# Kernel optimization log

Measured on AMD Instinct MI355X. Metric: run time of the kernel, lower is better.

## Reference

```python
import jax, jax.numpy as jnp
import numpy as np

N_NODES = 100000
N_EDGES = 3200000
D = 128
BN_EPS = 1e-5


def setup_inputs() -> dict:
    key = jax.random.key(0)
    k1, k2, k3, k4 = jax.random.split(key, 4)
    x = jax.random.normal(k1, (N_NODES, D), dtype=jnp.float32)
    edge_index = jax.random.randint(k2, (2, N_EDGES), 0, N_NODES, dtype=jnp.int64)
    # GCNConv linear weight, torch nn.Linear convention: [out_dim, in_dim]
    W = jax.random.normal(k3, (D, D), dtype=jnp.float32) * (1.0 / np.sqrt(D))
    # BatchNorm1d affine params
    gamma = jnp.ones((D,), dtype=jnp.float32) + 0.1 * jax.random.normal(k4, (D,), dtype=jnp.float32)
    beta = jnp.zeros((D,), dtype=jnp.float32)
    return {"x": x, "edge_index": edge_index, "W": W, "gamma": gamma, "beta": beta}


def reference(x, edge_index, W, gamma, beta):
    # GCNConv(bias=False, add_self_loops=False), then BN (batch stats), ReLU, skip-add.
    src, dst = edge_index[0], edge_index[1]
    n = x.shape[0]

    # linear transform: [N, D_out]
    h = x @ W.T

    # symmetric GCN normalization: deg over destination, norm = d^-1/2[src]*d^-1/2[dst]
    ones = jnp.ones((src.shape[0],), dtype=x.dtype)
    deg = jax.ops.segment_sum(ones, dst, num_segments=n)
    dinv = jnp.where(deg > 0, jax.lax.rsqrt(jnp.maximum(deg, 1.0)), 0.0)
    norm = dinv[src] * dinv[dst]  # [E]

    # gather-message-scatter: [E, D] -> [N, D]
    msg = h[src] * norm[:, None]
    agg = jax.ops.segment_sum(msg, dst, num_segments=n)

    # BatchNorm1d in training mode (batch statistics, biased variance)
    mean = jnp.mean(agg, axis=0)
    var = jnp.mean(jnp.square(agg - mean), axis=0)
    bn = (agg - mean) * jax.lax.rsqrt(var + BN_EPS) * gamma + beta

    # ReLU + residual skip (dims match)
    out = jax.nn.relu(bn) + x
    return out
```

## Files before the change

kernel.cpp:

```cpp
#include <hip/hip_runtime.h>
#include <hip/hip_bf16.h>
#include <cstdint>
#include <cstddef>

#define D 128
#define SBLK 512
#define SBBITS 10
#define NSB 128
#define TILE 2048

typedef __attribute__((ext_vector_type(8))) short short8;
typedef __attribute__((ext_vector_type(4))) float f32x4;

__device__ __forceinline__ unsigned short f2bf(float f) {
    union { float f; unsigned u; } v; v.f = f;
    unsigned r = v.u + 0x7FFF + ((v.u >> 16) & 1);
    return (unsigned short)(r >> 16);
}
__device__ __forceinline__ float bflo(unsigned p) {
    union { unsigned u; float f; } v; v.u = p << 16; return v.f;
}
__device__ __forceinline__ float bfhi(unsigned p) {
    union { unsigned u; float f; } v; v.u = p & 0xFFFF0000u; return v.f;
}

__global__ void k_detect(const unsigned* __restrict__ ei, int E, int* flag) {
    if (threadIdx.x == 0 && blockIdx.x == 0) {
        int n = E < 256 ? E : 256;
        int allz = 1;
        for (int k = 0; k < n; ++k) {
            if (ei[2 * k + 1] != 0u) { allz = 0; break; }
        }
        *flag = allz;
    }
}

__global__ void k_wcvt(const float* __restrict__ W, unsigned short* __restrict__ Wbf) {
    int i = blockIdx.x * 256 + threadIdx.x;
    if (i < D * D) Wbf[i] = f2bf(W[i]);
}

__global__ __launch_bounds__(256) void k_gemm(const float* __restrict__ x,
                                              const unsigned short* __restrict__ Wbf,
                                              unsigned short* __restrict__ h, int M) {
    int wave = threadIdx.x >> 6, lane = threadIdx.x & 63;
    int m0 = blockIdx.x * 64 + wave * 16;
    int lr = lane & 15;
    int lg = lane >> 4;
    f32x4 acc[8];
#pragma unroll
    for (int i = 0; i < 8; ++i) acc[i] = (f32x4){0.f, 0.f, 0.f, 0.f};

    int row = m0 + lr;
    int rowc = row < M ? row : M - 1;
    const float* xr = x + (size_t)rowc * D;

#pragma unroll
    for (int ks = 0; ks < 4; ++ks) {
        int k0 = ks * 32 + lg * 8;
        float4 a0 = *(const float4*)(xr + k0);
        float4 a1 = *(const float4*)(xr + k0 + 4);
        short8 af;
        af[0] = (short)f2bf(a0.x); af[1] = (short)f2bf(a0.y);
        af[2] = (short)f2bf(a0.z); af[3] = (short)f2bf(a0.w);
        af[4] = (short)f2bf(a1.x); af[5] = (short)f2bf(a1.y);
        af[6] = (short)f2bf(a1.z); af[7] = (short)f2bf(a1.w);
#pragma unroll
        for (int nt = 0; nt < 8; ++nt) {
            short8 bf = *(const short8*)(Wbf + (size_t)(nt * 16 + lr) * D + k0);
            acc[nt] = __builtin_amdgcn_mfma_f32_16x16x32_bf16(af, bf, acc[nt], 0, 0, 0);
        }
    }
#pragma unroll
    for (int nt = 0; nt < 8; ++nt) {
#pragma unroll
        for (int r = 0; r < 4; ++r) {
            int rr = m0 + lg * 4 + r;
            if (rr < M) h[(size_t)rr * D + nt * 16 + lr] = f2bf(acc[nt][r]);
        }
    }
}

__global__ __launch_bounds__(256) void k_bin(const int* __restrict__ ei, int E,
                                             const int* __restrict__ flagp,
                                             int* __restrict__ g_sbcnt,
                                             unsigned* __restrict__ binned, int C2) {
    __shared__ unsigned stage[TILE];
    __shared__ unsigned char ssb[TILE];
    __shared__ int hcnt[NSB], hoff[NSB], lcur[NSB], gbase[NSB];
    int f64 = *flagp;
    int t = threadIdx.x;
    int base = blockIdx.x * TILE;
    int cnt = E - base; if (cnt > TILE) cnt = TILE;

    if (t < NSB) hcnt[t] = 0;
    __syncthreads();

    unsigned ent[8]; int esb[8];
#pragma unroll
    for (int j = 0; j < 8; ++j) {
        int idx = j * 256 + t;
        esb[j] = -1;
        if (idx < cnt) {
            int e = base + idx;
            int s, d;
            if (f64) { s = ei[2 * e]; d = ei[2 * (E + e)]; }
            else     { s = ei[e];     d = ei[E + e]; }
            esb[j] = d >> SBBITS;
            ent[j] = (unsigned)s | ((unsigned)(d & ((1 << SBBITS) - 1)) << 17);
            atomicAdd(&hcnt[esb[j]], 1);
        }
    }
    __syncthreads();
    if (t < NSB) hoff[t] = hcnt[t];
    __syncthreads();
#pragma unroll
    for (int off = 1; off < NSB; off <<= 1) {
        int a = (t < NSB && t >= off) ? hoff[t - off] : 0;
        __syncthreads();
        if (t < NSB) hoff[t] += a;
        __syncthreads();
    }
    if (t < NSB) {
        int ex = hoff[t] - hcnt[t];
        lcur[t] = ex;
        hoff[t] = ex;
        gbase[t] = (hcnt[t] > 0) ? atomicAdd(&g_sbcnt[t], hcnt[t]) : 0;
    }
    __syncthreads();
#pragma unroll
    for (int j = 0; j < 8; ++j) {
        if (esb[j] >= 0) {
            int p = atomicAdd(&lcur[esb[j]], 1);
            stage[p] = ent[j];
            ssb[p] = (unsigned char)esb[j];
        }
    }
    __syncthreads();
    for (int i = t; i < cnt; i += 256) {
        int sb = ssb[i];
        int pos = gbase[sb] + (i - hoff[sb]);
        if (pos < C2) binned[(size_t)sb * C2 + pos] = stage[i];
    }
}

__global__ __launch_bounds__(1024) void k_fill2(const unsigned* __restrict__ binned, int C2,
                                                const int* __restrict__ g_sbcnt,
                                                int2* __restrict__ ronode,
                                                float* __restrict__ dinv,
                                                int* __restrict__ csrc, int N) {
    __shared__ int deg[1024];
    __shared__ int scn[1024];
    __shared__ int cur[1024];
    int b = blockIdx.x, t = threadIdx.x;
    int cnt = g_sbcnt[b]; if (cnt > C2) cnt = C2;
    const unsigned* ent = binned + (size_t)b * C2;

    deg[t] = 0;
    __syncthreads();
    for (int i = t; i < cnt; i += 1024) atomicAdd(&deg[ent[i] >> 17], 1);
    __syncthreads();
    scn[t] = deg[t];
    __syncthreads();
    for (int off = 1; off < 1024; off <<= 1) {
        int a = (t >= off) ? scn[t - off] : 0;
        __syncthreads();
        scn[t] += a;
        __syncthreads();
    }
    int ex = scn[t] - deg[t];
    cur[t] = ex;
    int node = (b << SBBITS) + t;
    if (node < N) {
        ronode[node] = make_int2(b * C2 + ex, deg[t]);
        dinv[node] = deg[t] > 0 ? rsqrtf((float)deg[t]) : 0.0f;
    }
    __syncthreads();
    for (int i = t; i < cnt; i += 1024) {
        unsigned e = ent[i];
        int pos = atomicAdd(&cur[e >> 17], 1);
        csrc[b * C2 + pos] = (int)(e & 0x1FFFF);
    }
}

__global__ __launch_bounds__(256) void k_agg(const unsigned* __restrict__ h,
                                             const int* __restrict__ csrc,
                                             const int2* __restrict__ ronode,
                                             const float* __restrict__ dinv,
                                             float2* __restrict__ out, int N) {
    int wave = threadIdx.x >> 6, lane = threadIdx.x & 63;
    int node = blockIdx.x * 4 + wave;
    if (node >= N) return;
    int2 ro = ronode[node];
    int beg = ro.x, end = ro.x + ro.y;
    float ax = 0.f, ay = 0.f;
    int i = beg;
    for (; i + 8 <= end; i += 8) {
        int s0 = csrc[i], s1 = csrc[i + 1], s2 = csrc[i + 2], s3 = csrc[i + 3];
        int s4 = csrc[i + 4], s5 = csrc[i + 5], s6 = csrc[i + 6], s7 = csrc[i + 7];
        unsigned p0 = h[(size_t)s0 * 64 + lane];
        unsigned p1 = h[(size_t)s1 * 64 + lane];
        unsigned p2 = h[(size_t)s2 * 64 + lane];
        unsigned p3 = h[(size_t)s3 * 64 + lane];
        unsigned p4 = h[(size_t)s4 * 64 + lane];
        unsigned p5 = h[(size_t)s5 * 64 + lane];
        unsigned p6 = h[(size_t)s6 * 64 + lane];
        unsigned p7 = h[(size_t)s7 * 64 + lane];
        float w0 = dinv[s0], w1 = dinv[s1], w2 = dinv[s2], w3 = dinv[s3];
        float w4 = dinv[s4], w5 = dinv[s5], w6 = dinv[s6], w7 = dinv[s7];
        ax += w0 * bflo(p0); ay += w0 * bfhi(p0);
        ax += w1 * bflo(p1); ay += w1 * bfhi(p1);
        ax += w2 * bflo(p2); ay += w2 * bfhi(p2);
        ax += w3 * bflo(p3); ay += w3 * bfhi(p3);
        ax += w4 * bflo(p4); ay += w4 * bfhi(p4);
        ax += w5 * bflo(p5); ay += w5 * bfhi(p5);
        ax += w6 * bflo(p6); ay += w6 * bfhi(p6);
        ax += w7 * bflo(p7); ay += w7 * bfhi(p7);
    }
    for (; i < end; ++i) {
        int s = csrc[i];
        float w = dinv[s];
        unsigned p = h[(size_t)s * 64 + lane];
        ax += w * bflo(p); ay += w * bfhi(p);
    }
    float sd = dinv[node];
    out[(size_t)node * 64 + lane] = make_float2(ax * sd, ay * sd);
}

__global__ __launch_bounds__(256) void k_stats(const float* __restrict__ agg,
                                               float* __restrict__ part, int N) {
    int t = threadIdx.x;
    int c = t & 127, half = t >> 7;
    float s = 0.f, q = 0.f;
    for (int r = blockIdx.x * 2 + half; r < N; r += SBLK * 2) {
        float v = agg[(size_t)r * 128 + c];
        s += v; q += v * v;
    }
    __shared__ float sh[512];
    sh[t] = s; sh[256 + t] = q;
    __syncthreads();
    if (t < 128) {
        part[blockIdx.x * 256 + t]       = sh[t] + sh[t + 128];
        part[blockIdx.x * 256 + 128 + t] = sh[256 + t] + sh[256 + t + 128];
    }
}

__global__ void k_params(const float* __restrict__ part, const float* __restrict__ gamma,
                         const float* __restrict__ beta, float* __restrict__ params, int N) {
    int t = threadIdx.x;
    float a = 0.f;
    for (int b = 0; b < SBLK; ++b) a += part[b * 256 + t];
    __shared__ float sh[256];
    sh[t] = a;
    __syncthreads();
    if (t < 128) {
        float mean = sh[t] / (float)N;
        float var = sh[128 + t] / (float)N - mean * mean;
        var = var > 0.f ? var : 0.f;
        float sc = gamma[t] * rsqrtf(var + 1e-5f);
        params[t] = sc;
        params[128 + t] = beta[t] - mean * sc;
    }
}

__global__ __launch_bounds__(256) void k_final(float4* __restrict__ out,
                                               const float4* __restrict__ x,
                                               const float* __restrict__ params, int n4) {
    const float4* p4 = (const float4*)params;
    for (int i = blockIdx.x * 256 + threadIdx.x; i < n4; i += gridDim.x * 256) {
        int c = i & 31;
        float4 s = p4[c], b = p4[32 + c];
        float4 v = out[i], xv = x[i];
        float4 r;
        r.x = fmaxf(v.x * s.x + b.x, 0.f) + xv.x;
        r.y = fmaxf(v.y * s.y + b.y, 0.f) + xv.y;
        r.z = fmaxf(v.z * s.z + b.z, 0.f) + xv.z;
        r.w = fmaxf(v.w * s.w + b.w, 0.f) + xv.w;
        out[i] = r;
    }
}

extern "C" void kernel_launch(void* const* d_in, const int* in_sizes, int n_in,
                              void* d_out, int out_size, void* d_ws, size_t ws_size,
                              hipStream_t stream) {
    const float* x     = (const float*)d_in[0];
    const int*   ei    = (const int*)d_in[1];
    const float* W     = (const float*)d_in[2];
    const float* gamma = (const float*)d_in[3];
    const float* beta  = (const float*)d_in[4];

    int N = in_sizes[0] / D;
    int E = in_sizes[1] / 2;
    int NSBu = (N + (1 << SBBITS) - 1) >> SBBITS;
    int avg = (E + NSBu - 1) / NSBu;
    int C2 = ((avg + 4096 + 63) / 64) * 64;

    char* ws = (char*)d_ws;
    size_t off = 0;
    auto alloc = [&](size_t bytes) { size_t o = off; off = (off + bytes + 255) & ~(size_t)255; return o; };

    unsigned short* h    = (unsigned short*)(ws + alloc((size_t)N * D * 2));
    int*      csrc   = (int*)     (ws + alloc((size_t)NSBu * C2 * 4));
    unsigned* binned = (unsigned*)(ws + alloc((size_t)NSBu * C2 * 4));
    int*      g_sbcnt= (int*)     (ws + alloc((size_t)NSB * 4));
    float*    dinv   = (float*)   (ws + alloc((size_t)N * 4));
    int2*     ronode = (int2*)    (ws + alloc((size_t)N * 8));
    float*    part   = (float*)   (ws + alloc((size_t)SBLK * 256 * 4));
    float*    params = (float*)   (ws + alloc(256 * 4));
    int*      flagp  = (int*)     (ws + alloc(4));
    unsigned short* Wbf = (unsigned short*)(ws + alloc((size_t)D * D * 2));

    float* outf = (float*)d_out;

    hipMemsetAsync(g_sbcnt, 0, (size_t)NSB * 4, stream);
    k_detect<<<1, 64, 0, stream>>>((const unsigned*)ei, E, flagp);
    k_wcvt<<<(D * D + 255) / 256, 256, 0, stream>>>(W, Wbf);
    k_gemm<<<(N + 63) / 64, 256, 0, stream>>>(x, Wbf, h, N);
    k_bin<<<(E + TILE - 1) / TILE, 256, 0, stream>>>(ei, E, flagp, g_sbcnt, binned, C2);
    k_fill2<<<NSBu, 1024, 0, stream>>>(binned, C2, g_sbcnt, ronode, dinv, csrc, N);
    k_agg<<<(N + 3) / 4, 256, 0, stream>>>((const unsigned*)h, csrc, ronode, dinv,
                                           (float2*)d_out, N);
    k_stats<<<SBLK, 256, 0, stream>>>(outf, part, N);
    k_params<<<1, 256, 0, stream>>>(part, gamma, beta, params, N);
    k_final<<<2048, 256, 0, stream>>>((float4*)d_out, (const float4*)x, params,
                                      (N * D) / 4);
}
```

Measured before the change: 396.9 us.

## Use finer dst superblocks, split-wave 8-byte gathers, and merge prep kernels

Shrinks destination superblocks from 1024 to 256 nodes, which gives 391 CSR fill blocks of 256 threads instead of 98 blocks of 1024. The binning histogram grows to 512 bins, scanned as pairs. The aggregation kernel now has each half-wave handle a different edge, with 8-byte gathers per lane, and combines the halves with a shuffle. This doubles the edges in flight per wave. The W conversion, format detection and counter zeroing are merged into one prep kernel to cut launches. The smaller slack C2 (avg+1024) raises the risk of overflow truncation on skewed degree distributions.

```diff
diff --git a/kernel.cpp b/kernel.cpp
--- a/kernel.cpp
+++ b/kernel.cpp
@@ -5,8 +5,8 @@
 
 #define D 128
 #define SBLK 512
-#define SBBITS 10
-#define NSB 128
+#define SBBITS 8
+#define NSB2 512
 #define TILE 2048
 
 typedef __attribute__((ext_vector_type(8))) short short8;
@@ -24,8 +24,15 @@
     union { unsigned u; float f; } v; v.u = p & 0xFFFF0000u; return v.f;
 }
 
-__global__ void k_detect(const unsigned* __restrict__ ei, int E, int* flag) {
-    if (threadIdx.x == 0 && blockIdx.x == 0) {
+__global__ __launch_bounds__(256) void k_prep(const unsigned* __restrict__ ei, int E,
+                                              int* __restrict__ flag,
+                                              const float* __restrict__ W,
+                                              unsigned short* __restrict__ Wbf,
+                                              int* __restrict__ g_sbcnt) {
+    int t = threadIdx.x, b = blockIdx.x;
+    int i = b * 256 + t;
+    if (i < D * D) Wbf[i] = f2bf(W[i]);
+    if (b == 0 && t == 0) {
         int n = E < 256 ? E : 256;
         int allz = 1;
         for (int k = 0; k < n; ++k) {
@@ -33,11 +40,7 @@
         }
         *flag = allz;
     }
-}
-
-__global__ void k_wcvt(const float* __restrict__ W, unsigned short* __restrict__ Wbf) {
-    int i = blockIdx.x * 256 + threadIdx.x;
-    if (i < D * D) Wbf[i] = f2bf(W[i]);
+    if (b == 63) { g_sbcnt[t] = 0; g_sbcnt[t + 256] = 0; }
 }
 
 __global__ __launch_bounds__(256) void k_gemm(const float* __restrict__ x,
@@ -86,14 +89,15 @@
                                              int* __restrict__ g_sbcnt,
                                              unsigned* __restrict__ binned, int C2) {
     __shared__ unsigned stage[TILE];
-    __shared__ unsigned char ssb[TILE];
-    __shared__ int hcnt[NSB], hoff[NSB], lcur[NSB], gbase[NSB];
+    __shared__ unsigned short ssb[TILE];
+    __shared__ int hcnt[NSB2], hoff[NSB2], lcur[NSB2], gbase[NSB2];
+    __shared__ int cpair[256];
     int f64 = *flagp;
     int t = threadIdx.x;
     int base = blockIdx.x * TILE;
     int cnt = E - base; if (cnt > TILE) cnt = TILE;
 
-    if (t < NSB) hcnt[t] = 0;
+    hcnt[t] = 0; hcnt[t + 256] = 0;
     __syncthreads();
 
     unsigned ent[8]; int esb[8];
@@ -112,20 +116,24 @@
         }
     }
     __syncthreads();
-    if (t < NSB) hoff[t] = hcnt[t];
-    __syncthreads();
-#pragma unroll
-    for (int off = 1; off < NSB; off <<= 1) {
-        int a = (t < NSB && t >= off) ? hoff[t - off] : 0;
+    cpair[t] = hcnt[2 * t] + hcnt[2 * t + 1];
+    __syncthreads();
+#pragma unroll
+    for (int off = 1; off < 256; off <<= 1) {
+        int a = (t >= off) ? cpair[t - off] : 0;
         __syncthreads();
-        if (t < NSB) hoff[t] += a;
+        cpair[t] += a;
         __syncthreads();
     }
-    if (t < NSB) {
-        int ex = hoff[t] - hcnt[t];
-        lcur[t] = ex;
-        hoff[t] = ex;
-        gbase[t] = (hcnt[t] > 0) ? atomicAdd(&g_sbcnt[t], hcnt[t]) : 0;
+    {
+        int pairsum = hcnt[2 * t] + hcnt[2 * t + 1];
+        int ex2 = cpair[t] - pairsum;
+        hoff[2 * t] = ex2;
+        hoff[2 * t + 1] = ex2 + hcnt[2 * t];
+        lcur[2 * t] = ex2;
+        lcur[2 * t + 1] = ex2 + hcnt[2 * t];
+        gbase[2 * t]     = hcnt[2 * t]     > 0 ? atomicAdd(&g_sbcnt[2 * t],     hcnt[2 * t])     : 0;
+        gbase[2 * t + 1] = hcnt[2 * t + 1] > 0 ? atomicAdd(&g_sbcnt[2 * t + 1], hcnt[2 * t + 1]) : 0;
     }
     __syncthreads();
 #pragma unroll
@@ -133,7 +141,7 @@
         if (esb[j] >= 0) {
             int p = atomicAdd(&lcur[esb[j]], 1);
             stage[p] = ent[j];
-            ssb[p] = (unsigned char)esb[j];
+            ssb[p] = (unsigned short)esb[j];
         }
     }
     __syncthreads();
@@ -144,25 +152,26 @@
     }
 }
 
-__global__ __launch_bounds__(1024) void k_fill2(const unsigned* __restrict__ binned, int C2,
-                                                const int* __restrict__ g_sbcnt,
-                                                int2* __restrict__ ronode,
-                                                float* __restrict__ dinv,
-                                                int* __restrict__ csrc, int N) {
-    __shared__ int deg[1024];
-    __shared__ int scn[1024];
-    __shared__ int cur[1024];
+__global__ __launch_bounds__(256) void k_fill2(const unsigned* __restrict__ binned, int C2,
+                                               const int* __restrict__ g_sbcnt,
+                                               int2* __restrict__ ronode,
+                                               float* __restrict__ dinv,
+                                               int* __restrict__ csrc, int N) {
+    __shared__ int deg[256];
+    __shared__ int scn[256];
+    __shared__ int cur[256];
     int b = blockIdx.x, t = threadIdx.x;
     int cnt = g_sbcnt[b]; if (cnt > C2) cnt = C2;
     const unsigned* ent = binned + (size_t)b * C2;
 
     deg[t] = 0;
     __syncthreads();
-    for (int i = t; i < cnt; i += 1024) atomicAdd(&deg[ent[i] >> 17], 1);
+    for (int i = t; i < cnt; i += 256) atomicAdd(&deg[ent[i] >> 17], 1);
     __syncthreads();
     scn[t] = deg[t];
     __syncthreads();
-    for (int off = 1; off < 1024; off <<= 1) {
+#pragma unroll
+    for (int off = 1; off < 256; off <<= 1) {
         int a = (t >= off) ? scn[t - off] : 0;
         __syncthreads();
         scn[t] += a;
@@ -176,55 +185,62 @@
         dinv[node] = deg[t] > 0 ? rsqrtf((float)deg[t]) : 0.0f;
     }
     __syncthreads();
-    for (int i = t; i < cnt; i += 1024) {
+    for (int i = t; i < cnt; i += 256) {
         unsigned e = ent[i];
         int pos = atomicAdd(&cur[e >> 17], 1);
         csrc[b * C2 + pos] = (int)(e & 0x1FFFF);
     }
 }
 
-__global__ __launch_bounds__(256) void k_agg(const unsigned* __restrict__ h,
+__global__ __launch_bounds__(256) void k_agg(const unsigned long long* __restrict__ h,
                                              const int* __restrict__ csrc,
                                              const int2* __restrict__ ronode,
                                              const float* __restrict__ dinv,
-                                             float2* __restrict__ out, int N) {
+                                             float4* __restrict__ out, int N) {
     int wave = threadIdx.x >> 6, lane = threadIdx.x & 63;
     int node = blockIdx.x * 4 + wave;
     if (node >= N) return;
+    int half = lane >> 5, lq = lane & 31;
     int2 ro = ronode[node];
     int beg = ro.x, end = ro.x + ro.y;
-    float ax = 0.f, ay = 0.f;
+    float a0 = 0.f, a1 = 0.f, a2 = 0.f, a3 = 0.f;
     int i = beg;
-    for (; i + 8 <= end; i += 8) {
-        int s0 = csrc[i], s1 = csrc[i + 1], s2 = csrc[i + 2], s3 = csrc[i + 3];
-        int s4 = csrc[i + 4], s5 = csrc[i + 5], s6 = csrc[i + 6], s7 = csrc[i + 7];
-        unsigned p0 = h[(size_t)s0 * 64 + lane];
-        unsigned p1 = h[(size_t)s1 * 64 + lane];
-        unsigned p2 = h[(size_t)s2 * 64 + lane];
-        unsigned p3 = h[(size_t)s3 * 64 + lane];
-        unsigned p4 = h[(size_t)s4 * 64 + lane];
-        unsigned p5 = h[(size_t)s5 * 64 + lane];
-        unsigned p6 = h[(size_t)s6 * 64 + lane];
-        unsigned p7 = h[(size_t)s7 * 64 + lane];
-        float w0 = dinv[s0], w1 = dinv[s1], w2 = dinv[s2], w3 = dinv[s3];
-        float w4 = dinv[s4], w5 = dinv[s5], w6 = dinv[s6], w7 = dinv[s7];
-        ax += w0 * bflo(p0); ay += w0 * bfhi(p0);
-        ax += w1 * bflo(p1); ay += w1 * bfhi(p1);
-        ax += w2 * bflo(p2); ay += w2 * bfhi(p2);
-        ax += w3 * bflo(p3); ay += w3 * bfhi(p3);
-        ax += w4 * bflo(p4); ay += w4 * bfhi(p4);
-        ax += w5 * bflo(p5); ay += w5 * bfhi(p5);
-        ax += w6 * bflo(p6); ay += w6 * bfhi(p6);
-        ax += w7 * bflo(p7); ay += w7 * bfhi(p7);
-    }
-    for (; i < end; ++i) {
+    for (; i + 16 <= end; i += 16) {
+#pragma unroll
+        for (int p = 0; p < 8; ++p) {
+            int e = i + 2 * p + half;
+            int s = csrc[e];
+            float w = dinv[s];
+            unsigned long long pk = h[(size_t)s * 32 + lq];
+            unsigned lo = (unsigned)pk, hi = (unsigned)(pk >> 32);
+            a0 += w * bflo(lo); a1 += w * bfhi(lo);
+            a2 += w * bflo(hi); a3 += w * bfhi(hi);
+        }
+    }
+    for (; i + 2 <= end; i += 2) {
+        int e = i + half;
+        int s = csrc[e];
+        float w = dinv[s];
+        unsigned long long pk = h[(size_t)s * 32 + lq];
+        unsigned lo = (unsigned)pk, hi = (unsigned)(pk >> 32);
+        a0 += w * bflo(lo); a1 += w * bfhi(lo);
+        a2 += w * bflo(hi); a3 += w * bfhi(hi);
+    }
+    if (i < end) {
         int s = csrc[i];
-        float w = dinv[s];
-        unsigned p = h[(size_t)s * 64 + lane];
-        ax += w * bflo(p); ay += w * bfhi(p);
-    }
+        float w = half ? 0.f : dinv[s];
+        unsigned long long pk = h[(size_t)s * 32 + lq];
+        unsigned lo = (unsigned)pk, hi = (unsigned)(pk >> 32);
+        a0 += w * bflo(lo); a1 += w * bfhi(lo);
+        a2 += w * bflo(hi); a3 += w * bfhi(hi);
+    }
+    a0 += __shfl_xor(a0, 32);
+    a1 += __shfl_xor(a1, 32);
+    a2 += __shfl_xor(a2, 32);
+    a3 += __shfl_xor(a3, 32);
     float sd = dinv[node];
-    out[(size_t)node * 64 + lane] = make_float2(ax * sd, ay * sd);
+    if (half == 0)
+        out[(size_t)node * 32 + lq] = make_float4(a0 * sd, a1 * sd, a2 * sd, a3 * sd);
 }
 
 __global__ __launch_bounds__(256) void k_stats(const float* __restrict__ agg,
@@ -293,7 +309,7 @@
     int E = in_sizes[1] / 2;
     int NSBu = (N + (1 << SBBITS) - 1) >> SBBITS;
     int avg = (E + NSBu - 1) / NSBu;
-    int C2 = ((avg + 4096 + 63) / 64) * 64;
+    int C2 = ((avg + 1024 + 63) / 64) * 64;
 
     char* ws = (char*)d_ws;
     size_t off = 0;
@@ -302,7 +318,7 @@
     unsigned short* h    = (unsigned short*)(ws + alloc((size_t)N * D * 2));
     int*      csrc   = (int*)     (ws + alloc((size_t)NSBu * C2 * 4));
     unsigned* binned = (unsigned*)(ws + alloc((size_t)NSBu * C2 * 4));
-    int*      g_sbcnt= (int*)     (ws + alloc((size_t)NSB * 4));
+    int*      g_sbcnt= (int*)     (ws + alloc((size_t)NSB2 * 4));
     float*    dinv   = (float*)   (ws + alloc((size_t)N * 4));
     int2*     ronode = (int2*)    (ws + alloc((size_t)N * 8));
     float*    part   = (float*)   (ws + alloc((size_t)SBLK * 256 * 4));
@@ -312,14 +328,12 @@
 
     float* outf = (float*)d_out;
 
-    hipMemsetAsync(g_sbcnt, 0, (size_t)NSB * 4, stream);
-    k_detect<<<1, 64, 0, stream>>>((const unsigned*)ei, E, flagp);
-    k_wcvt<<<(D * D + 255) / 256, 256, 0, stream>>>(W, Wbf);
+    k_prep<<<64, 256, 0, stream>>>((const unsigned*)ei, E, flagp, W, Wbf, g_sbcnt);
     k_gemm<<<(N + 63) / 64, 256, 0, stream>>>(x, Wbf, h, N);
     k_bin<<<(E + TILE - 1) / TILE, 256, 0, stream>>>(ei, E, flagp, g_sbcnt, binned, C2);
-    k_fill2<<<NSBu, 1024, 0, stream>>>(binned, C2, g_sbcnt, ronode, dinv, csrc, N);
-    k_agg<<<(N + 3) / 4, 256, 0, stream>>>((const unsigned*)h, csrc, ronode, dinv,
-                                           (float2*)d_out, N);
+    k_fill2<<<NSBu, 256, 0, stream>>>(binned, C2, g_sbcnt, ronode, dinv, csrc, N);
+    k_agg<<<(N + 3) / 4, 256, 0, stream>>>((const unsigned long long*)h, csrc, ronode, dinv,
+                                           (float4*)d_out, N);
     k_stats<<<SBLK, 256, 0, stream>>>(outf, part, N);
     k_params<<<1, 256, 0, stream>>>(part, gamma, beta, params, N);
     k_final<<<2048, 256, 0, stream>>>((float4*)d_out, (const float4*)x, params,
```

Measured after the change: 413.8 us. +4.3%, slower.
